# Optimization experiments

Measured on AMD Instinct MI355X. Metric: run time of the kernel, lower is better.

## Reference

```python
import jax, jax.numpy as jnp
import numpy as np


def setup_inputs() -> dict:
    key = jax.random.key(0)
    ks = jax.random.split(key, 6)
    B, S, E, H = 8, 2048, 1024, 64
    scale = 1.0 / np.sqrt(E)
    return {
        "query": jax.random.normal(ks[0], (B, S, E), dtype=jnp.float32),
        "key": jax.random.normal(ks[1], (B, S, E), dtype=jnp.float32),
        "value": jax.random.normal(ks[2], (B, S, E), dtype=jnp.float32),
        "Wq": jax.random.normal(ks[3], (E, H), dtype=jnp.float32) * scale,
        "bq": jnp.zeros((H,), dtype=jnp.float32),
        "Wk": jax.random.normal(ks[4], (E, H), dtype=jnp.float32) * scale,
        "bk": jnp.zeros((H,), dtype=jnp.float32),
        "Wv": jax.random.normal(ks[5], (E, H), dtype=jnp.float32) * scale,
        "bv": jnp.zeros((H,), dtype=jnp.float32),
    }


def reference(query, key, value, Wq, bq, Wk, bk, Wv, bv):
    # Linear projections: [B,S,E] @ [E,H] + [H] -> [B,S,H]
    q = jnp.einsum("bse,eh->bsh", query, Wq) + bq
    k = jnp.einsum("bse,eh->bsh", key, Wk) + bk
    v = jnp.einsum("bse,eh->bsh", value, Wv) + bv
    head_dim = q.shape[-1]
    # scores [B,S,S], softmax over last axis, then weighted sum of values
    scores = jnp.einsum("bqh,bkh->bqk", q, k) / jnp.sqrt(
        jnp.asarray(head_dim, dtype=q.dtype)
    )
    attn = jax.nn.softmax(scores, axis=-1)
    return jnp.einsum("bqk,bkh->bqh", attn, v)
```

## Files before the change

### kernel.cpp

```cpp
#include <hip/hip_runtime.h>
#include <math.h>

#define BB 8
#define SS 2048
#define EE 1024
#define HH 64
#define MM (BB * SS)

typedef unsigned short u16;
typedef __attribute__((ext_vector_type(8))) short short8;
typedef __attribute__((ext_vector_type(4))) float floatx4;

__device__ __forceinline__ u16 f2bf(float f) {
    union { float f; unsigned u; } a; a.f = f;
    unsigned r = a.u + 0x7fffu + ((a.u >> 16) & 1u);
    return (u16)(r >> 16);
}

__device__ __forceinline__ void split2(float f0, float f1, unsigned& hp, unsigned& lp) {
    union { float f; unsigned u; } a0, a1, h0, h1, l0, l1;
    a0.f = f0; a1.f = f1;
    h0.u = a0.u & 0xffff0000u;
    h1.u = a1.u & 0xffff0000u;
    l0.f = f0 - h0.f;
    l1.f = f1 - h1.f;
    hp = __builtin_amdgcn_perm(a1.u, a0.u, 0x07060302u);
    lp = __builtin_amdgcn_perm(l1.u, l0.u, 0x07060302u);
}

#define WP_MAT 131072

__global__ __launch_bounds__(512) void pack_w(
    const float* __restrict__ W0, const float* __restrict__ W1, const float* __restrict__ W2,
    u16* __restrict__ Wp)
{
    const int which = blockIdx.y;
    const float* __restrict__ W = (which == 0) ? W0 : (which == 1) ? W1 : W2;
    const float scale = (which == 0) ? 0.125f : 1.0f;
    const int t    = blockIdx.x;
    const int tid  = threadIdx.x;
    const int ks   = tid >> 8;
    const int nt   = (tid >> 6) & 3;
    const int lane = tid & 63;
    const int n    = lane & 15;
    const int g    = lane >> 4;

    const int k0 = t * 64 + ks * 32 + g * 8;
    const int c  = nt * 16 + n;

    float e[8];
    #pragma unroll
    for (int j = 0; j < 8; ++j) e[j] = W[(size_t)(k0 + j) * HH + c] * scale;

    unsigned hp[4], lp[4];
    #pragma unroll
    for (int i = 0; i < 4; ++i) split2(e[2 * i], e[2 * i + 1], hp[i], lp[i]);

    u16* dst = Wp + (size_t)which * WP_MAT
                  + ((size_t)(t * 8 + ks * 4 + nt) * 2) * 512 + lane * 8;
    *(uint4*)dst         = (uint4){hp[0], hp[1], hp[2], hp[3]};
    *(uint4*)(dst + 512) = (uint4){lp[0], lp[1], lp[2], lp[3]};
}

#define PCH 8

__global__ __launch_bounds__(256, 6) void proj_mfma(
    const float* __restrict__ A0, const float* __restrict__ A1, const float* __restrict__ A2,
    const u16* __restrict__ Wp,
    const float* __restrict__ b0, const float* __restrict__ b1, const float* __restrict__ b2,
    u16* __restrict__ o0, u16* __restrict__ o1, u16* __restrict__ o2)
{
    const int which = blockIdx.y;
    const float* __restrict__ A    = (which == 0) ? A0 : (which == 1) ? A1 : A2;
    const float* __restrict__ bias = (which == 0) ? b0 : (which == 1) ? b1 : b2;
    u16* __restrict__ out          = (which == 0) ? o0 : (which == 1) ? o1 : o2;
    const float bscale = (which == 0) ? 0.125f : 1.0f;

    __shared__ float Cb[2][16][68];

    const int tid  = threadIdx.x;
    const int lane = tid & 63;
    const int wave = tid >> 6;
    const int kh   = wave & 1;
    const int rg   = wave >> 1;
    const int n    = lane & 15;
    const int g    = lane >> 4;
    const int row0 = blockIdx.x * 32 + rg * 16;

    const float* __restrict__ ap = A + (size_t)(row0 + n) * EE + kh * (PCH * 64) + g * 8;
    const u16* __restrict__ wpb = Wp + (size_t)which * WP_MAT + (size_t)kh * PCH * 8192 + lane * 8;

    floatx4 acc[4];
    #pragma unroll
    for (int nt = 0; nt < 4; ++nt) acc[nt] = (floatx4){0.f, 0.f, 0.f, 0.f};

    float4 av[2][4];
    #pragma unroll
    for (int s = 0; s < 2; ++s) {
        const float* p = ap + s * 64;
        av[s][0] = *(const float4*)(p + 0);
        av[s][1] = *(const float4*)(p + 4);
        av[s][2] = *(const float4*)(p + 32);
        av[s][3] = *(const float4*)(p + 36);
    }

    for (int t = 0; t < PCH; ++t) {
        const int cur = t & 1;

        short8 ah[2], al[2];
        #pragma unroll
        for (int ks = 0; ks < 2; ++ks) {
            unsigned hp0, lp0, hp1, lp1, hp2, lp2, hp3, lp3;
            split2(av[cur][ks * 2].x,     av[cur][ks * 2].y,     hp0, lp0);
            split2(av[cur][ks * 2].z,     av[cur][ks * 2].w,     hp1, lp1);
            split2(av[cur][ks * 2 + 1].x, av[cur][ks * 2 + 1].y, hp2, lp2);
            split2(av[cur][ks * 2 + 1].z, av[cur][ks * 2 + 1].w, hp3, lp3);
            union { uint4 u; short8 s; } ch, cl;
            ch.u = (uint4){hp0, hp1, hp2, hp3};
            cl.u = (uint4){lp0, lp1, lp2, lp3};
            ah[ks] = ch.s; al[ks] = cl.s;
        }

        if (t + 2 < PCH) {
            const float* p = ap + (t + 2) * 64;
            av[cur][0] = *(const float4*)(p + 0);
            av[cur][1] = *(const float4*)(p + 4);
            av[cur][2] = *(const float4*)(p + 32);
            av[cur][3] = *(const float4*)(p + 36);
        }

        const u16* wpc = wpb + t * 8192;
        #pragma unroll
        for (int ks = 0; ks < 2; ++ks)
            #pragma unroll
            for (int nt = 0; nt < 4; ++nt) {
                const short8 whf = *(const short8*)(wpc + ((ks * 4 + nt) * 2 + 0) * 512);
                const short8 wlf = *(const short8*)(wpc + ((ks * 4 + nt) * 2 + 1) * 512);
                acc[nt] = __builtin_amdgcn_mfma_f32_16x16x32_bf16(ah[ks], whf, acc[nt], 0, 0, 0);
                acc[nt] = __builtin_amdgcn_mfma_f32_16x16x32_bf16(al[ks], whf, acc[nt], 0, 0, 0);
                acc[nt] = __builtin_amdgcn_mfma_f32_16x16x32_bf16(ah[ks], wlf, acc[nt], 0, 0, 0);
            }
    }

    if (kh == 1) {
        #pragma unroll
        for (int nt = 0; nt < 4; ++nt)
            #pragma unroll
            for (int r = 0; r < 4; ++r)
                Cb[rg][g * 4 + r][nt * 16 + n] = acc[nt][r];
    }
    __syncthreads();
    if (kh == 0) {
        #pragma unroll
        for (int nt = 0; nt < 4; ++nt) {
            const float bv = bias[nt * 16 + n] * bscale;
            #pragma unroll
            for (int r = 0; r < 4; ++r) {
                const int row = row0 + g * 4 + r;
                const float v = acc[nt][r] + Cb[rg][g * 4 + r][nt * 16 + n] + bv;
                out[(size_t)row * HH + nt * 16 + n] = f2bf(v);
            }
        }
    }
}

__global__ __launch_bounds__(256) void flash_mfma(
    const u16* __restrict__ qp, const u16* __restrict__ kp,
    const u16* __restrict__ vp, float* __restrict__ out)
{
    __shared__ __align__(16) u16 Ks[2][64 * 64];
    __shared__ __align__(16) u16 Vt[2][64 * 64];
    __shared__ __align__(16) u16 Pw[4][16 * 72];

    const int b    = blockIdx.y;
    const int q0   = blockIdx.x * 32;
    const int tid  = threadIdx.x;
    const int lane = tid & 63;
    const int wave = tid >> 6;
    const int wq   = wave & 1;
    const int ks   = wave >> 1;
    const int n    = lane & 15;
    const int g    = lane >> 4;

    const u16* qrow = qp + ((size_t)b * SS + q0 + wq * 16 + n) * HH;
    const short8 qa0 = *(const short8*)(qrow + g * 8);
    const short8 qa1 = *(const short8*)(qrow + 32 + g * 8);

    floatx4 Oa[4];
    #pragma unroll
    for (int ht = 0; ht < 4; ++ht) Oa[ht] = (floatx4){0.f, 0.f, 0.f, 0.f};
    float m_i[4], l_i[4];
    #pragma unroll
    for (int r = 0; r < 4; ++r) { m_i[r] = -1e30f; l_i[r] = 0.f; }

    const u16* kb = kp + (size_t)b * SS * HH;
    const u16* vb = vp + (size_t)b * SS * HH;

    const int jK0 = tid >> 3, jK1 = 32 + (tid >> 3), cs = tid & 7;
    const int jV  = (tid & 15) * 4, hV = (tid >> 4) * 4;

    short8  kr0, kr1;
    ushort4 vr0, vr1, vr2, vr3;

    kr0 = *(const short8*)(kb + (size_t)jK0 * HH + cs * 8);
    kr1 = *(const short8*)(kb + (size_t)jK1 * HH + cs * 8);
    vr0 = *(const ushort4*)(vb + (size_t)(jV + 0) * HH + hV);
    vr1 = *(const ushort4*)(vb + (size_t)(jV + 1) * HH + hV);
    vr2 = *(const ushort4*)(vb + (size_t)(jV + 2) * HH + hV);
    vr3 = *(const ushort4*)(vb + (size_t)(jV + 3) * HH + hV);
    {
        *(short8*)&Ks[0][jK0 * 64 + ((cs ^ (jK0 & 7)) << 3)] = kr0;
        *(short8*)&Ks[0][jK1 * 64 + ((cs ^ (jK1 & 7)) << 3)] = kr1;
        const u16* a0 = (const u16*)&vr0; const u16* a1 = (const u16*)&vr1;
        const u16* a2 = (const u16*)&vr2; const u16* a3 = (const u16*)&vr3;
        #pragma unroll
        for (int i = 0; i < 4; ++i) {
            const int h = hV + i;
            ushort4 w; w.x = a0[i]; w.y = a1[i]; w.z = a2[i]; w.w = a3[i];
            *(ushort4*)((char*)&Vt[0][0] + h * 128 + (((jV >> 3) ^ (h & 7)) << 4) + ((jV & 4) << 1)) = w;
        }
    }
    __syncthreads();

    for (int t = 0; t < SS / 64; ++t) {
        const int cur = t & 1;

        if (t + 1 < SS / 64) {
            const size_t kt = (size_t)(t + 1) * 64;
            kr0 = *(const short8*)(kb + (kt + jK0) * HH + cs * 8);
            kr1 = *(const short8*)(kb + (kt + jK1) * HH + cs * 8);
            vr0 = *(const ushort4*)(vb + (kt + jV + 0) * HH + hV);
            vr1 = *(const ushort4*)(vb + (kt + jV + 1) * HH + hV);
            vr2 = *(const ushort4*)(vb + (kt + jV + 2) * HH + hV);
            vr3 = *(const ushort4*)(vb + (kt + jV + 3) * HH + hV);
        }

        floatx4 S[2];
        #pragma unroll
        for (int nt = 0; nt < 2; ++nt) {
            const int j = ks * 32 + nt * 16 + n;
            const short8 kf0 = *(const short8*)&Ks[cur][j * 64 + (((0 + g) ^ (j & 7)) << 3)];
            const short8 kf1 = *(const short8*)&Ks[cur][j * 64 + (((4 + g) ^ (j & 7)) << 3)];
            floatx4 a = (floatx4){0.f, 0.f, 0.f, 0.f};
            a = __builtin_amdgcn_mfma_f32_16x16x32_bf16(qa0, kf0, a, 0, 0, 0);
            a = __builtin_amdgcn_mfma_f32_16x16x32_bf16(qa1, kf1, a, 0, 0, 0);
            S[nt] = a;
        }

        float mx[4];
        #pragma unroll
        for (int r = 0; r < 4; ++r) mx[r] = -1e30f;
        #pragma unroll
        for (int nt = 0; nt < 2; ++nt)
            #pragma unroll
            for (int r = 0; r < 4; ++r)
                mx[r] = fmaxf(mx[r], S[nt][r]);
        #pragma unroll
        for (int off = 8; off >= 1; off >>= 1)
            #pragma unroll
            for (int r = 0; r < 4; ++r)
                mx[r] = fmaxf(mx[r], __shfl_xor(mx[r], off, 64));

        float alpha[4], ps[4];
        #pragma unroll
        for (int r = 0; r < 4; ++r) {
            const float Mn = fmaxf(m_i[r], mx[r]);
            alpha[r] = __expf(m_i[r] - Mn);
            m_i[r]   = Mn;
            ps[r]    = 0.f;
        }
        float p[2][4];
        #pragma unroll
        for (int nt = 0; nt < 2; ++nt)
            #pragma unroll
            for (int r = 0; r < 4; ++r) {
                p[nt][r] = __expf(S[nt][r] - m_i[r]);
                ps[r] += p[nt][r];
            }
        #pragma unroll
        for (int off = 8; off >= 1; off >>= 1)
            #pragma unroll
            for (int r = 0; r < 4; ++r)
                ps[r] += __shfl_xor(ps[r], off, 64);
        #pragma unroll
        for (int r = 0; r < 4; ++r) l_i[r] = l_i[r] * alpha[r] + ps[r];
        #pragma unroll
        for (int ht = 0; ht < 4; ++ht)
            #pragma unroll
            for (int r = 0; r < 4; ++r) Oa[ht][r] *= alpha[r];

        #pragma unroll
        for (int nt = 0; nt < 2; ++nt)
            #pragma unroll
            for (int r = 0; r < 4; ++r)
                Pw[wave][(g * 4 + r) * 72 + nt * 16 + n] = f2bf(p[nt][r]);
        const short8 pa = *(const short8*)&Pw[wave][n * 72 + g * 8];

        #pragma unroll
        for (int ht = 0; ht < 4; ++ht) {
            const int h = ht * 16 + n;
            const short8 vf = *(const short8*)((const char*)&Vt[cur][0] + h * 128 +
                                               ((((ks << 2) + g) ^ (h & 7)) << 4));
            Oa[ht] = __builtin_amdgcn_mfma_f32_16x16x32_bf16(pa, vf, Oa[ht], 0, 0, 0);
        }

        if (t + 1 < SS / 64) {
            const int nx = cur ^ 1;
            *(short8*)&Ks[nx][jK0 * 64 + ((cs ^ (jK0 & 7)) << 3)] = kr0;
            *(short8*)&Ks[nx][jK1 * 64 + ((cs ^ (jK1 & 7)) << 3)] = kr1;
            const u16* a0 = (const u16*)&vr0; const u16* a1 = (const u16*)&vr1;
            const u16* a2 = (const u16*)&vr2; const u16* a3 = (const u16*)&vr3;
            #pragma unroll
            for (int i = 0; i < 4; ++i) {
                const int h = hV + i;
                ushort4 w; w.x = a0[i]; w.y = a1[i]; w.z = a2[i]; w.w = a3[i];
                *(ushort4*)((char*)&Vt[nx][0] + h * 128 + (((jV >> 3) ^ (h & 7)) << 4) + ((jV & 4) << 1)) = w;
            }
        }
        __syncthreads();
    }

    float* Cb = (float*)&Ks[0][0];
    float* Cm = Cb + 2 * 16 * 68;
    float* Cl = Cm + 32;
    if (ks == 1) {
        #pragma unroll
        for (int ht = 0; ht < 4; ++ht)
            #pragma unroll
            for (int r = 0; r < 4; ++r)
                Cb[(wq * 16 + g * 4 + r) * 68 + ht * 16 + n] = Oa[ht][r];
        if (n == 0)
            #pragma unroll
            for (int r = 0; r < 4; ++r) {
                Cm[wq * 16 + g * 4 + r] = m_i[r];
                Cl[wq * 16 + g * 4 + r] = l_i[r];
            }
    }
    __syncthreads();
    if (ks == 0) {
        float a0v[4], a1v[4], linv[4];
        #pragma unroll
        for (int r = 0; r < 4; ++r) {
            const int m = g * 4 + r;
            const float m1 = Cm[wq * 16 + m], l1 = Cl[wq * 16 + m];
            const float M  = fmaxf(m_i[r], m1);
            const float e0 = __expf(m_i[r] - M), e1 = __expf(m1 - M);
            a0v[r] = e0; a1v[r] = e1;
            linv[r] = 1.f / (l_i[r] * e0 + l1 * e1);
        }
        #pragma unroll
        for (int ht = 0; ht < 4; ++ht)
            #pragma unroll
            for (int r = 0; r < 4; ++r) {
                const float o1 = Cb[(wq * 16 + g * 4 + r) * 68 + ht * 16 + n];
                const float v  = (Oa[ht][r] * a0v[r] + o1 * a1v[r]) * linv[r];
                out[((size_t)b * SS + q0 + wq * 16 + g * 4 + r) * HH + ht * 16 + n] = v;
            }
    }
}

extern "C" void kernel_launch(void* const* d_in, const int* in_sizes, int n_in,
                              void* d_out, int out_size, void* d_ws, size_t ws_size,
                              hipStream_t stream) {
    const float* query = (const float*)d_in[0];
    const float* key   = (const float*)d_in[1];
    const float* value = (const float*)d_in[2];
    const float* Wq    = (const float*)d_in[3];
    const float* bq    = (const float*)d_in[4];
    const float* Wk    = (const float*)d_in[5];
    const float* bk    = (const float*)d_in[6];
    const float* Wv    = (const float*)d_in[7];
    const float* bv    = (const float*)d_in[8];
    float* out = (float*)d_out;

    u16* qp = (u16*)d_ws;
    u16* kp = qp + (size_t)MM * HH;
    u16* vp = kp + (size_t)MM * HH;
    u16* Wp = vp + (size_t)MM * HH;

    dim3 wgrid(EE / 64, 3);
    pack_w<<<wgrid, 512, 0, stream>>>(Wq, Wk, Wv, Wp);

    dim3 pgrid(MM / 32, 3);
    proj_mfma<<<pgrid, 256, 0, stream>>>(query, key, value,
                                         Wp,
                                         bq, bk, bv,
                                         qp, kp, vp);

    dim3 agrid(SS / 32, BB);
    flash_mfma<<<agrid, 256, 0, stream>>>(qp, kp, vp, out);
}
```

Measured before the change: 291.2 us.

## Stage packed weights in LDS via async copies, drop split-K in projection

Result: slower. 327.5 us (+12.5%).

```diff
diff --git a/kernel.cpp b/kernel.cpp
--- a/kernel.cpp
+++ b/kernel.cpp
@@ -26,6 +26,12 @@
     l1.f = f1 - h1.f;
     hp = __builtin_amdgcn_perm(a1.u, a0.u, 0x07060302u);
     lp = __builtin_amdgcn_perm(l1.u, l0.u, 0x07060302u);
+}
+
+__device__ __forceinline__ void async_copy16(const u16* g, u16* l) {
+    __builtin_amdgcn_global_load_lds(
+        (const __attribute__((address_space(1))) unsigned*)g,
+        (__attribute__((address_space(3))) unsigned*)l, 16, 0, 0);
 }
 
 #define WP_MAT 131072
@@ -62,9 +68,9 @@
     *(uint4*)(dst + 512) = (uint4){lp[0], lp[1], lp[2], lp[3]};
 }
 
-#define PCH 8
-
-__global__ __launch_bounds__(256, 6) void proj_mfma(
+#define PCH 16
+
+__global__ __launch_bounds__(256) void proj_mfma(
     const float* __restrict__ A0, const float* __restrict__ A1, const float* __restrict__ A2,
     const u16* __restrict__ Wp,
     const float* __restrict__ b0, const float* __restrict__ b1, const float* __restrict__ b2,
@@ -76,19 +82,17 @@
     u16* __restrict__ out          = (which == 0) ? o0 : (which == 1) ? o1 : o2;
     const float bscale = (which == 0) ? 0.125f : 1.0f;
 
-    __shared__ float Cb[2][16][68];
+    __shared__ __align__(16) u16 Wb[2][8192];
 
     const int tid  = threadIdx.x;
     const int lane = tid & 63;
     const int wave = tid >> 6;
-    const int kh   = wave & 1;
-    const int rg   = wave >> 1;
     const int n    = lane & 15;
     const int g    = lane >> 4;
-    const int row0 = blockIdx.x * 32 + rg * 16;
-
-    const float* __restrict__ ap = A + (size_t)(row0 + n) * EE + kh * (PCH * 64) + g * 8;
-    const u16* __restrict__ wpb = Wp + (size_t)which * WP_MAT + (size_t)kh * PCH * 8192 + lane * 8;
+    const int row0 = blockIdx.x * 64;
+
+    const float* __restrict__ ap = A + (size_t)(row0 + wave * 16 + n) * EE + g * 8;
+    const u16* __restrict__ wpb = Wp + (size_t)which * WP_MAT;
 
     floatx4 acc[4];
     #pragma unroll
@@ -103,9 +107,24 @@
         av[s][2] = *(const float4*)(p + 32);
         av[s][3] = *(const float4*)(p + 36);
     }
+    {
+        const u16* src = wpb + wave * 2048 + lane * 8;
+        #pragma unroll
+        for (int i = 0; i < 4; ++i)
+            async_copy16(src + i * 512, &Wb[0][wave * 2048 + i * 512]);
+    }
+    __syncthreads();
 
     for (int t = 0; t < PCH; ++t) {
         const int cur = t & 1;
+
+        if (t + 1 < PCH) {
+            const u16* src = wpb + (size_t)(t + 1) * 8192 + wave * 2048 + lane * 8;
+            u16* dst = &Wb[cur ^ 1][wave * 2048];
+            #pragma unroll
+            for (int i = 0; i < 4; ++i)
+                async_copy16(src + i * 512, dst + i * 512);
+        }
 
         short8 ah[2], al[2];
         #pragma unroll
@@ -129,37 +148,28 @@
             av[cur][3] = *(const float4*)(p + 36);
         }
 
-        const u16* wpc = wpb + t * 8192;
         #pragma unroll
         for (int ks = 0; ks < 2; ++ks)
             #pragma unroll
             for (int nt = 0; nt < 4; ++nt) {
-                const short8 whf = *(const short8*)(wpc + ((ks * 4 + nt) * 2 + 0) * 512);
-                const short8 wlf = *(const short8*)(wpc + ((ks * 4 + nt) * 2 + 1) * 512);
+                const int f = ks * 4 + nt;
+                const short8 whf = *(const short8*)&Wb[cur][f * 1024 + lane * 8];
+                const short8 wlf = *(const short8*)&Wb[cur][f * 1024 + 512 + lane * 8];
                 acc[nt] = __builtin_amdgcn_mfma_f32_16x16x32_bf16(ah[ks], whf, acc[nt], 0, 0, 0);
                 acc[nt] = __builtin_amdgcn_mfma_f32_16x16x32_bf16(al[ks], whf, acc[nt], 0, 0, 0);
                 acc[nt] = __builtin_amdgcn_mfma_f32_16x16x32_bf16(ah[ks], wlf, acc[nt], 0, 0, 0);
             }
-    }
-
-    if (kh == 1) {
-        #pragma unroll
-        for (int nt = 0; nt < 4; ++nt)
-            #pragma unroll
-            for (int r = 0; r < 4; ++r)
-                Cb[rg][g * 4 + r][nt * 16 + n] = acc[nt][r];
-    }
-    __syncthreads();
-    if (kh == 0) {
-        #pragma unroll
-        for (int nt = 0; nt < 4; ++nt) {
-            const float bv = bias[nt * 16 + n] * bscale;
-            #pragma unroll
-            for (int r = 0; r < 4; ++r) {
-                const int row = row0 + g * 4 + r;
-                const float v = acc[nt][r] + Cb[rg][g * 4 + r][nt * 16 + n] + bv;
-                out[(size_t)row * HH + nt * 16 + n] = f2bf(v);
-            }
+
+        __syncthreads();
+    }
+
+    #pragma unroll
+    for (int nt = 0; nt < 4; ++nt) {
+        const float bv = bias[nt * 16 + n] * bscale;
+        #pragma unroll
+        for (int r = 0; r < 4; ++r) {
+            const int row = row0 + wave * 16 + g * 4 + r;
+            out[(size_t)row * HH + nt * 16 + n] = f2bf(acc[nt][r] + bv);
         }
     }
 }
@@ -381,7 +391,7 @@
     dim3 wgrid(EE / 64, 3);
     pack_w<<<wgrid, 512, 0, stream>>>(Wq, Wk, Wv, Wp);
 
-    dim3 pgrid(MM / 32, 3);
+    dim3 pgrid(MM / 64, 3);
     proj_mfma<<<pgrid, 256, 0, stream>>>(query, key, value,
                                          Wp,
                                          bq, bk, bv,
```
